# Performance work log

Hardware: AMD Instinct MI355X
Metric: run time of the kernel (lower is better)

Reference implementation:

```python
import jax, jax.numpy as jnp
import numpy as np

B, H, M, C = 64, 8, 1024, 128
MID = 64  # mid_dims[1]


def setup_inputs() -> dict:
    key = jax.random.key(0)
    ks = jax.random.split(key, 11)
    inp = {
        "query": jax.random.normal(ks[0], (B, H, C), jnp.float32),
        "key_feat": jax.random.normal(ks[1], (B, H, M, C), jnp.float32),
        "att_mask": jax.random.randint(ks[2], (B, M), 0, 2, jnp.int32),
        "value1": jax.random.normal(ks[3], (B, H, C), jnp.float32),
        "value2": jax.random.normal(ks[4], (B, H, M, C), jnp.float32),
        # MH_Linear params (kaiming-uniform-ish scale)
        "w_basic": jax.random.uniform(ks[5], (H, C, MID), jnp.float32, -1, 1) / np.sqrt(C),
        "b_basic": jax.random.uniform(ks[6], (H, MID), jnp.float32, -1, 1) / np.sqrt(C),
        "w_last": jax.random.uniform(ks[7], (H, MID, 1), jnp.float32, -1, 1) / np.sqrt(MID),
        "b_last": jax.random.uniform(ks[8], (H, 1), jnp.float32, -1, 1) / np.sqrt(MID),
        "w_last2": jax.random.uniform(ks[9], (H, MID, C), jnp.float32, -1, 1) / np.sqrt(MID),
        "b_last2": jax.random.uniform(ks[10], (H, C), jnp.float32, -1, 1) / np.sqrt(MID),
    }
    return inp


def reference(query, key_feat, att_mask, value1, value2,
              w_basic, b_basic, w_last, b_last, w_last2, b_last2):
    # att_map: [B,H,M,C] -> basic projection [B,H,M,MID] + ReLU (dropout is eval/no-op)
    att_map = query[:, :, None, :] * key_feat
    att_map = jnp.einsum('bhmi,hio->bhmo', att_map, w_basic) + b_basic[None, :, None, :]
    att_map = jax.nn.relu(att_map)

    mask_f = att_mask.astype(att_map.dtype)            # [B,M]
    m_ext = mask_f[:, None, :, None]                    # [B,1,M,1]
    # masked mean-pool over spatial dim M -> [B,H,MID]
    att_map_pool = jnp.sum(att_map * m_ext, axis=-2) / jnp.sum(m_ext, axis=-2)

    # spatial attention logits -> [B,H,M]
    alpha_spatial = (jnp.einsum('bhmi,hio->bhmo', att_map, w_last)
                     + b_last[None, :, None, :]).squeeze(-1)
    alpha_spatial = jnp.where(att_mask[:, None, :] == 0, jnp.float32(-1e9), alpha_spatial)
    alpha_spatial = jax.nn.softmax(alpha_spatial, axis=-1)

    # attend values: [B,H,M] x [B,H,M,C] -> [B,H,C]
    v2 = jnp.einsum('bhm,bhmd->bhd', alpha_spatial, value2)

    # channel gate: [B,H,MID] -> [B,H,C]
    alpha_channel = jax.nn.sigmoid(
        jnp.einsum('bhi,hio->bho', att_map_pool, w_last2) + b_last2[None])

    return value1 * v2 * alpha_channel
```

## Files before the change

### kernel.cpp

```cpp
#include <hip/hip_runtime.h>

#define NB   64
#define NH   8
#define NM   1024
#define NC   128
#define NMID 64
#define NT   256
#define TM   32
#define NTILES (NM / TM)
#define RWS  136
#define KFS  136

typedef __attribute__((ext_vector_type(8))) short s16x8;
typedef __attribute__((ext_vector_type(4))) short s16x4;
typedef __attribute__((ext_vector_type(4))) float f32x4;

__device__ __forceinline__ short f2bf(float x) {
    union { float f; unsigned u; } v; v.f = x;
    unsigned r = (v.u + 0x7fffu + ((v.u >> 16) & 1u)) >> 16;
    return (short)r;
}
__device__ __forceinline__ float bf2f(short s) {
    union { unsigned u; float f; } v; v.u = ((unsigned)(unsigned short)s) << 16;
    return v.f;
}

__global__ __launch_bounds__(NT, 2)
void scatt_kernel(const float* __restrict__ query,
                  const float* __restrict__ key_feat,
                  const int*   __restrict__ att_mask,
                  const float* __restrict__ value1,
                  const float* __restrict__ value2,
                  const float* __restrict__ w_basic,
                  const float* __restrict__ b_basic,
                  const float* __restrict__ w_last,
                  const float* __restrict__ b_last,
                  const float* __restrict__ w_last2,
                  const float* __restrict__ b_last2,
                  float* __restrict__ out)
{
    const int bh   = blockIdx.x;
    const int b    = bh >> 3;
    const int h    = bh & 7;
    const int t    = threadIdx.x;
    const int lane = t & 63;
    const int w    = t >> 6;
    const int oh   = w & 1;
    const int rt   = w >> 1;
    const int ln15 = lane & 15;
    const int lq   = lane >> 4;

    __shared__ short rwT_hi[NMID * RWS];
    __shared__ short rwT_lo[NMID * RWS];
    __shared__ short kf_hi[TM * KFS];
    __shared__ short kf_lo[TM * KFS];
    __shared__ float logith[2][NM];
    __shared__ float poolp[4][32];
    __shared__ float pool_s[NMID];
    __shared__ float v2part[8][NC];
    __shared__ float red[8];
    __shared__ float sscal[4];

    const float* kf  = key_feat + (size_t)bh * NM * NC;
    const float* v2g = value2   + (size_t)bh * NM * NC;

    float4 st[4];
    const float4* kf4 = (const float4*)kf;
    #pragma unroll
    for (int r = 0; r < 4; ++r) st[r] = kf4[r * NT + t];

    {
        const float* wb = w_basic + (size_t)h * NC * NMID;
        const float* qp = query + bh * NC;
        #pragma unroll 4
        for (int r = 0; r < 32; ++r) {
            const int f = r * NT + t;
            const int o = f & 63;
            const int i = f >> 6;
            const float x = qp[i] * wb[f];
            const short hi = f2bf(x);
            rwT_hi[o * RWS + i] = hi;
            rwT_lo[o * RWS + i] = f2bf(x - bf2f(hi));
        }
    }
    __syncthreads();

    s16x8 Bh[2][4], Bl[2][4];
    #pragma unroll
    for (int otl = 0; otl < 2; ++otl) {
        const int o = oh * 32 + otl * 16 + ln15;
        #pragma unroll
        for (int ks = 0; ks < 4; ++ks) {
            const int off = o * RWS + ks * 32 + lq * 8;
            Bh[otl][ks] = *(const s16x8*)&rwT_hi[off];
            Bl[otl][ks] = *(const s16x8*)&rwT_lo[off];
        }
    }

    const int o_0 = oh * 32 + ln15;
    const int o_1 = o_0 + 16;
    const float bb0 = b_basic[h * NMID + o_0];
    const float bb1 = b_basic[h * NMID + o_1];
    const float wl0 = w_last[h * NMID + o_0];
    const float wl1 = w_last[h * NMID + o_1];
    const float bl  = b_last[h];

    float pool0 = 0.f, pool1 = 0.f;
    const int abase = (rt * 16 + ln15) * KFS + lq * 8;

    #pragma unroll 1
    for (int tile = 0; tile < NTILES; ++tile) {
        if (tile) __syncthreads();
        #pragma unroll
        for (int r = 0; r < 4; ++r) {
            const int g   = r * NT + t;
            const int row = g >> 5;
            const int gc  = g & 31;
            const float v0 = st[r].x, v1 = st[r].y, v2 = st[r].z, v3 = st[r].w;
            s16x4 h4, l4;
            short hh;
            hh = f2bf(v0); h4[0] = hh; l4[0] = f2bf(v0 - bf2f(hh));
            hh = f2bf(v1); h4[1] = hh; l4[1] = f2bf(v1 - bf2f(hh));
            hh = f2bf(v2); h4[2] = hh; l4[2] = f2bf(v2 - bf2f(hh));
            hh = f2bf(v3); h4[3] = hh; l4[3] = f2bf(v3 - bf2f(hh));
            *(s16x4*)&kf_hi[row * KFS + gc * 4] = h4;
            *(s16x4*)&kf_lo[row * KFS + gc * 4] = l4;
        }
        __syncthreads();
        if (tile + 1 < NTILES) {
            #pragma unroll
            for (int r = 0; r < 4; ++r)
                st[r] = kf4[(size_t)(tile + 1) * (TM * NC / 4) + r * NT + t];
        }

        f32x4 acc0 = {0.f, 0.f, 0.f, 0.f};
        f32x4 acc1 = {0.f, 0.f, 0.f, 0.f};
        #pragma unroll
        for (int ks = 0; ks < 4; ++ks) {
            const s16x8 Ah = *(const s16x8*)&kf_hi[abase + ks * 32];
            const s16x8 Al = *(const s16x8*)&kf_lo[abase + ks * 32];
            acc0 = __builtin_amdgcn_mfma_f32_16x16x32_bf16(Ah, Bh[0][ks], acc0, 0, 0, 0);
            acc1 = __builtin_amdgcn_mfma_f32_16x16x32_bf16(Ah, Bh[1][ks], acc1, 0, 0, 0);
            acc0 = __builtin_amdgcn_mfma_f32_16x16x32_bf16(Al, Bh[0][ks], acc0, 0, 0, 0);
            acc1 = __builtin_amdgcn_mfma_f32_16x16x32_bf16(Al, Bh[1][ks], acc1, 0, 0, 0);
            acc0 = __builtin_amdgcn_mfma_f32_16x16x32_bf16(Ah, Bl[0][ks], acc0, 0, 0, 0);
            acc1 = __builtin_amdgcn_mfma_f32_16x16x32_bf16(Ah, Bl[1][ks], acc1, 0, 0, 0);
        }

        const int mbase = tile * TM + rt * 16 + lq * 4;
        float c4[4];
        #pragma unroll
        for (int reg = 0; reg < 4; ++reg) {
            const int m = mbase + reg;
            const float mvf = (float)att_mask[b * NM + m];
            const float y0 = fmaxf(acc0[reg] + bb0, 0.f);
            const float y1 = fmaxf(acc1[reg] + bb1, 0.f);
            pool0 = fmaf(mvf, y0, pool0);
            pool1 = fmaf(mvf, y1, pool1);
            c4[reg] = fmaf(y0, wl0, y1 * wl1);
        }
        #pragma unroll
        for (int reg = 0; reg < 4; ++reg) {
            #pragma unroll
            for (int s = 1; s < 16; s <<= 1) c4[reg] += __shfl_xor(c4[reg], s, 64);
        }
        if (ln15 == 0) {
            #pragma unroll
            for (int reg = 0; reg < 4; ++reg) logith[oh][mbase + reg] = c4[reg];
        }
    }

    pool0 += __shfl_xor(pool0, 16, 64); pool0 += __shfl_xor(pool0, 32, 64);
    pool1 += __shfl_xor(pool1, 16, 64); pool1 += __shfl_xor(pool1, 32, 64);
    if (lane < 16) { poolp[w][lane] = pool0; poolp[w][16 + lane] = pool1; }
    __syncthreads();

    float lmax = -1e30f, csum = 0.f;
    for (int m = t; m < NM; m += NT) {
        const int mv = att_mask[b * NM + m];
        float lg = logith[0][m] + logith[1][m] + bl;
        lg = mv ? lg : -1e9f;
        logith[0][m] = lg;
        lmax = fmaxf(lmax, lg);
        csum += (float)mv;
    }
    #pragma unroll
    for (int s = 32; s > 0; s >>= 1) {
        lmax = fmaxf(lmax, __shfl_xor(lmax, s, 64));
        csum += __shfl_xor(csum, s, 64);
    }
    if (lane == 0) { red[w] = lmax; red[4 + w] = csum; }
    __syncthreads();
    if (t == 0) {
        sscal[0] = fmaxf(fmaxf(red[0], red[1]), fmaxf(red[2], red[3]));
        sscal[2] = red[4] + red[5] + red[6] + red[7];
    }
    __syncthreads();
    const float mx  = sscal[0];
    const float cnt = sscal[2];
    if (t < NMID) {
        const int ohp = t >> 5, j = t & 31;
        pool_s[t] = (poolp[ohp][j] + poolp[ohp + 2][j]) / cnt;
    }
    float esum = 0.f;
    for (int m = t; m < NM; m += NT) {
        const float e = __expf(logith[0][m] - mx);
        logith[0][m] = e;
        esum += e;
    }
    #pragma unroll
    for (int s = 32; s > 0; s >>= 1) esum += __shfl_xor(esum, s, 64);
    if (lane == 0) red[w] = esum;
    __syncthreads();
    if (t == 0) sscal[1] = red[0] + red[1] + red[2] + red[3];
    __syncthreads();
    const float inv_sum = 1.f / sscal[1];

    const int d4 = t & 31;
    const int mg = t >> 5;
    float4 acc = make_float4(0.f, 0.f, 0.f, 0.f);
    const float4* v24 = (const float4*)v2g;
    #pragma unroll 4
    for (int m0 = 0; m0 < NM; m0 += 8) {
        const int m = m0 + mg;
        const float a = logith[0][m];
        const float4 v = v24[(size_t)m * 32 + d4];
        acc.x = fmaf(a, v.x, acc.x);
        acc.y = fmaf(a, v.y, acc.y);
        acc.z = fmaf(a, v.z, acc.z);
        acc.w = fmaf(a, v.w, acc.w);
    }
    ((float4*)&v2part[mg][0])[d4] = acc;
    __syncthreads();

    if (t < NC) {
        float v2d = 0.f;
        #pragma unroll
        for (int g = 0; g < 8; ++g) v2d += v2part[g][t];
        v2d *= inv_sum;
        float accd = b_last2[h * NC + t];
        const float* wl2 = w_last2 + (size_t)h * NMID * NC + t;
        #pragma unroll 8
        for (int o = 0; o < NMID; ++o)
            accd = fmaf(pool_s[o], wl2[(size_t)o * NC], accd);
        const float ach = 1.f / (1.f + __expf(-accd));
        out[bh * NC + t] = value1[bh * NC + t] * v2d * ach;
    }
}

extern "C" void kernel_launch(void* const* d_in, const int* in_sizes, int n_in,
                              void* d_out, int out_size, void* d_ws, size_t ws_size,
                              hipStream_t stream) {
    (void)in_sizes; (void)n_in; (void)out_size; (void)d_ws; (void)ws_size;
    const float* query    = (const float*)d_in[0];
    const float* key_feat = (const float*)d_in[1];
    const int*   att_mask = (const int*)d_in[2];
    const float* value1   = (const float*)d_in[3];
    const float* value2   = (const float*)d_in[4];
    const float* w_basic  = (const float*)d_in[5];
    const float* b_basic  = (const float*)d_in[6];
    const float* w_last   = (const float*)d_in[7];
    const float* b_last   = (const float*)d_in[8];
    const float* w_last2  = (const float*)d_in[9];
    const float* b_last2  = (const float*)d_in[10];
    float* outp = (float*)d_out;

    scatt_kernel<<<dim3(NB * NH), dim3(NT), 0, stream>>>(
        query, key_feat, att_mask, value1, value2,
        w_basic, b_basic, w_last, b_last, w_last2, b_last2, outp);
}
```

Measured before the change: 519.0 us.

## Fuse online softmax and value2 accumulation into the key_feat tile loop

The separate softmax and value2 passes after the main loop are replaced by an online (running max and sum) softmax computed per 32-row tile, and each tile's value2 rows are loaded and accumulated inside that loop. Loads of value2 and key_feat are issued one tile ahead so they overlap with the MFMA work. The attention mask is staged once into shared memory. The intent is to remove the second sequential streaming phase and overlap both input streams, at the cost of more registers, an extra barrier per tile, and per-tile rescaling of the accumulators.

```diff
diff --git a/kernel.cpp b/kernel.cpp
--- a/kernel.cpp
+++ b/kernel.cpp
@@ -10,6 +10,7 @@
 #define NTILES (NM / TM)
 #define RWS  136
 #define KFS  136
+#define TGRAN (TM * NC / 4)
 
 typedef __attribute__((ext_vector_type(8))) short s16x8;
 typedef __attribute__((ext_vector_type(4))) short s16x4;
@@ -24,6 +25,24 @@
     union { unsigned u; float f; } v; v.u = ((unsigned)(unsigned short)s) << 16;
     return v.f;
 }
+
+#define STAGE_KF(ST) do {                                                   \
+    _Pragma("unroll")                                                       \
+    for (int r_ = 0; r_ < 4; ++r_) {                                        \
+        const int g_   = r_ * NT + t;                                       \
+        const int row_ = g_ >> 5;                                           \
+        const int gc_  = g_ & 31;                                           \
+        const float a0 = (ST)[r_].x, a1 = (ST)[r_].y,                       \
+                    a2 = (ST)[r_].z, a3 = (ST)[r_].w;                       \
+        s16x4 h4_, l4_; short hh_;                                          \
+        hh_ = f2bf(a0); h4_[0] = hh_; l4_[0] = f2bf(a0 - bf2f(hh_));        \
+        hh_ = f2bf(a1); h4_[1] = hh_; l4_[1] = f2bf(a1 - bf2f(hh_));        \
+        hh_ = f2bf(a2); h4_[2] = hh_; l4_[2] = f2bf(a2 - bf2f(hh_));        \
+        hh_ = f2bf(a3); h4_[3] = hh_; l4_[3] = f2bf(a3 - bf2f(hh_));        \
+        *(s16x4*)&kf_hi[row_ * KFS + gc_ * 4] = h4_;                        \
+        *(s16x4*)&kf_lo[row_ * KFS + gc_ * 4] = l4_;                        \
+    }                                                                       \
+} while (0)
 
 __global__ __launch_bounds__(NT, 2)
 void scatt_kernel(const float* __restrict__ query,
@@ -49,25 +68,43 @@
     const int rt   = w >> 1;
     const int ln15 = lane & 15;
     const int lq   = lane >> 4;
+    const int mg   = t >> 5;
+    const int d4   = t & 31;
+    const int half = lane & 32;
 
     __shared__ short rwT_hi[NMID * RWS];
     __shared__ short rwT_lo[NMID * RWS];
     __shared__ short kf_hi[TM * KFS];
     __shared__ short kf_lo[TM * KFS];
-    __shared__ float logith[2][NM];
+    __shared__ float maskf[NM];
+    __shared__ float logp[2][TM];
     __shared__ float poolp[4][32];
     __shared__ float pool_s[NMID];
     __shared__ float v2part[8][NC];
     __shared__ float red[8];
-    __shared__ float sscal[4];
-
-    const float* kf  = key_feat + (size_t)bh * NM * NC;
-    const float* v2g = value2   + (size_t)bh * NM * NC;
-
-    float4 st[4];
+    __shared__ float csum_s;
+
+    const float*  kf  = key_feat + (size_t)bh * NM * NC;
+    const float*  v2g = value2   + (size_t)bh * NM * NC;
     const float4* kf4 = (const float4*)kf;
-    #pragma unroll
-    for (int r = 0; r < 4; ++r) st[r] = kf4[r * NT + t];
+    const float4* v24 = (const float4*)v2g;
+
+    float4 stA[4], stV[4];
+    #pragma unroll
+    for (int r = 0; r < 4; ++r) stA[r] = kf4[r * NT + t];
+    #pragma unroll
+    for (int r = 0; r < 4; ++r) stV[r] = v24[r * NT + t];
+
+    float cs = 0.f;
+    #pragma unroll
+    for (int m = t; m < NM; m += NT) {
+        const int mv = att_mask[b * NM + m];
+        maskf[m] = (float)mv;
+        cs += (float)mv;
+    }
+    #pragma unroll
+    for (int sh = 32; sh > 0; sh >>= 1) cs += __shfl_xor(cs, sh, 64);
+    if (lane == 0) red[w] = cs;
 
     {
         const float* wb = w_basic + (size_t)h * NC * NMID;
@@ -84,6 +121,7 @@
         }
     }
     __syncthreads();
+    if (t == 0) csum_s = red[0] + red[1] + red[2] + red[3];
 
     s16x8 Bh[2][4], Bl[2][4];
     #pragma unroll
@@ -106,33 +144,18 @@
     const float bl  = b_last[h];
 
     float pool0 = 0.f, pool1 = 0.f;
+    f32x4 accd = {0.f, 0.f, 0.f, 0.f};
+    float mx_run = -1e30f;
+    float s_run  = 0.f;
     const int abase = (rt * 16 + ln15) * KFS + lq * 8;
+
+    STAGE_KF(stA);
+    #pragma unroll
+    for (int r = 0; r < 4; ++r) stA[r] = kf4[TGRAN + r * NT + t];
+    __syncthreads();
 
     #pragma unroll 1
     for (int tile = 0; tile < NTILES; ++tile) {
-        if (tile) __syncthreads();
-        #pragma unroll
-        for (int r = 0; r < 4; ++r) {
-            const int g   = r * NT + t;
-            const int row = g >> 5;
-            const int gc  = g & 31;
-            const float v0 = st[r].x, v1 = st[r].y, v2 = st[r].z, v3 = st[r].w;
-            s16x4 h4, l4;
-            short hh;
-            hh = f2bf(v0); h4[0] = hh; l4[0] = f2bf(v0 - bf2f(hh));
-            hh = f2bf(v1); h4[1] = hh; l4[1] = f2bf(v1 - bf2f(hh));
-            hh = f2bf(v2); h4[2] = hh; l4[2] = f2bf(v2 - bf2f(hh));
-            hh = f2bf(v3); h4[3] = hh; l4[3] = f2bf(v3 - bf2f(hh));
-            *(s16x4*)&kf_hi[row * KFS + gc * 4] = h4;
-            *(s16x4*)&kf_lo[row * KFS + gc * 4] = l4;
-        }
-        __syncthreads();
-        if (tile + 1 < NTILES) {
-            #pragma unroll
-            for (int r = 0; r < 4; ++r)
-                st[r] = kf4[(size_t)(tile + 1) * (TM * NC / 4) + r * NT + t];
-        }
-
         f32x4 acc0 = {0.f, 0.f, 0.f, 0.f};
         f32x4 acc1 = {0.f, 0.f, 0.f, 0.f};
         #pragma unroll
@@ -147,12 +170,11 @@
             acc1 = __builtin_amdgcn_mfma_f32_16x16x32_bf16(Ah, Bl[1][ks], acc1, 0, 0, 0);
         }
 
-        const int mbase = tile * TM + rt * 16 + lq * 4;
+        const int rbase = rt * 16 + lq * 4;
         float c4[4];
         #pragma unroll
         for (int reg = 0; reg < 4; ++reg) {
-            const int m = mbase + reg;
-            const float mvf = (float)att_mask[b * NM + m];
+            const float mvf = maskf[tile * TM + rbase + reg];
             const float y0 = fmaxf(acc0[reg] + bb0, 0.f);
             const float y1 = fmaxf(acc1[reg] + bb1, 0.f);
             pool0 = fmaf(mvf, y0, pool0);
@@ -162,88 +184,79 @@
         #pragma unroll
         for (int reg = 0; reg < 4; ++reg) {
             #pragma unroll
-            for (int s = 1; s < 16; s <<= 1) c4[reg] += __shfl_xor(c4[reg], s, 64);
+            for (int sh = 1; sh < 16; sh <<= 1) c4[reg] += __shfl_xor(c4[reg], sh, 64);
         }
         if (ln15 == 0) {
             #pragma unroll
-            for (int reg = 0; reg < 4; ++reg) logith[oh][mbase + reg] = c4[reg];
+            for (int reg = 0; reg < 4; ++reg) logp[oh][rbase + reg] = c4[reg];
+        }
+        __syncthreads();
+
+        const int lrow = lane & 31;
+        float lg = logp[0][lrow] + logp[1][lrow] + bl;
+        lg = (maskf[tile * TM + lrow] != 0.f) ? lg : -1e9f;
+        float tmax = lg;
+        #pragma unroll
+        for (int sh = 1; sh <= 16; sh <<= 1) tmax = fmaxf(tmax, __shfl_xor(tmax, sh, 64));
+        const float nmx = fmaxf(mx_run, tmax);
+        const float fre = __expf(mx_run - nmx);
+        const float e   = __expf(lg - nmx);
+        float es = e;
+        #pragma unroll
+        for (int sh = 1; sh <= 16; sh <<= 1) es += __shfl_xor(es, sh, 64);
+        s_run = s_run * fre + es;
+        mx_run = nmx;
+
+        float ek[4];
+        #pragma unroll
+        for (int k = 0; k < 4; ++k) ek[k] = __shfl(e, half + mg + 8 * k, 64);
+
+        accd = accd * fre;
+        #pragma unroll
+        for (int k = 0; k < 4; ++k) {
+            accd[0] = fmaf(ek[k], stV[k].x, accd[0]);
+            accd[1] = fmaf(ek[k], stV[k].y, accd[1]);
+            accd[2] = fmaf(ek[k], stV[k].z, accd[2]);
+            accd[3] = fmaf(ek[k], stV[k].w, accd[3]);
+        }
+        if (tile + 1 < NTILES) {
+            #pragma unroll
+            for (int r = 0; r < 4; ++r)
+                stV[r] = v24[(size_t)(tile + 1) * TGRAN + r * NT + t];
+        }
+
+        if (tile + 1 < NTILES) STAGE_KF(stA);
+        __syncthreads();
+        if (tile + 2 < NTILES) {
+            #pragma unroll
+            for (int r = 0; r < 4; ++r)
+                stA[r] = kf4[(size_t)(tile + 2) * TGRAN + r * NT + t];
         }
     }
 
     pool0 += __shfl_xor(pool0, 16, 64); pool0 += __shfl_xor(pool0, 32, 64);
     pool1 += __shfl_xor(pool1, 16, 64); pool1 += __shfl_xor(pool1, 32, 64);
     if (lane < 16) { poolp[w][lane] = pool0; poolp[w][16 + lane] = pool1; }
-    __syncthreads();
-
-    float lmax = -1e30f, csum = 0.f;
-    for (int m = t; m < NM; m += NT) {
-        const int mv = att_mask[b * NM + m];
-        float lg = logith[0][m] + logith[1][m] + bl;
-        lg = mv ? lg : -1e9f;
-        logith[0][m] = lg;
-        lmax = fmaxf(lmax, lg);
-        csum += (float)mv;
-    }
-    #pragma unroll
-    for (int s = 32; s > 0; s >>= 1) {
-        lmax = fmaxf(lmax, __shfl_xor(lmax, s, 64));
-        csum += __shfl_xor(csum, s, 64);
-    }
-    if (lane == 0) { red[w] = lmax; red[4 + w] = csum; }
-    __syncthreads();
-    if (t == 0) {
-        sscal[0] = fmaxf(fmaxf(red[0], red[1]), fmaxf(red[2], red[3]));
-        sscal[2] = red[4] + red[5] + red[6] + red[7];
-    }
-    __syncthreads();
-    const float mx  = sscal[0];
-    const float cnt = sscal[2];
+    ((float4*)&v2part[mg][0])[d4] = make_float4(accd[0], accd[1], accd[2], accd[3]);
+    __syncthreads();
+
     if (t < NMID) {
         const int ohp = t >> 5, j = t & 31;
-        pool_s[t] = (poolp[ohp][j] + poolp[ohp + 2][j]) / cnt;
-    }
-    float esum = 0.f;
-    for (int m = t; m < NM; m += NT) {
-        const float e = __expf(logith[0][m] - mx);
-        logith[0][m] = e;
-        esum += e;
-    }
-    #pragma unroll
-    for (int s = 32; s > 0; s >>= 1) esum += __shfl_xor(esum, s, 64);
-    if (lane == 0) red[w] = esum;
-    __syncthreads();
-    if (t == 0) sscal[1] = red[0] + red[1] + red[2] + red[3];
-    __syncthreads();
-    const float inv_sum = 1.f / sscal[1];
-
-    const int d4 = t & 31;
-    const int mg = t >> 5;
-    float4 acc = make_float4(0.f, 0.f, 0.f, 0.f);
-    const float4* v24 = (const float4*)v2g;
-    #pragma unroll 4
-    for (int m0 = 0; m0 < NM; m0 += 8) {
-        const int m = m0 + mg;
-        const float a = logith[0][m];
-        const float4 v = v24[(size_t)m * 32 + d4];
-        acc.x = fmaf(a, v.x, acc.x);
-        acc.y = fmaf(a, v.y, acc.y);
-        acc.z = fmaf(a, v.z, acc.z);
-        acc.w = fmaf(a, v.w, acc.w);
-    }
-    ((float4*)&v2part[mg][0])[d4] = acc;
+        pool_s[t] = (poolp[ohp][j] + poolp[ohp + 2][j]) / csum_s;
+    }
     __syncthreads();
 
     if (t < NC) {
         float v2d = 0.f;
         #pragma unroll
         for (int g = 0; g < 8; ++g) v2d += v2part[g][t];
-        v2d *= inv_sum;
-        float accd = b_last2[h * NC + t];
+        v2d /= s_run;
+        float accg = b_last2[h * NC + t];
         const float* wl2 = w_last2 + (size_t)h * NMID * NC + t;
         #pragma unroll 8
         for (int o = 0; o < NMID; ++o)
-            accd = fmaf(pool_s[o], wl2[(size_t)o * NC], accd);
-        const float ach = 1.f / (1.f + __expf(-accd));
+            accg = fmaf(pool_s[o], wl2[(size_t)o * NC], accg);
+        const float ach = 1.f / (1.f + __expf(-accg));
         out[bh * NC + t] = value1[bh * NC + t] * v2d * ach;
     }
 }
```

Result: no change. 528.7 us (+1.9%).
